# Performance work log

Measured on AMD Instinct MI355X. Metric: run time of the kernel, lower is better.

## Reference

```python
import jax, jax.numpy as jnp
import numpy as np

LABEL_SMOOTHING = 0.1
K_SLOPE = 5.0
N, D = 8192, 256


def setup_inputs() -> dict:
    key = jax.random.key(0)
    k1, k2, k3 = jax.random.split(key, 3)
    return {
        "image_features1": jax.random.normal(k1, (N, D), dtype=jnp.float32),
        "image_features2": jax.random.normal(k2, (N, D), dtype=jnp.float32),
        "logit_scale": jnp.asarray(14.2857, dtype=jnp.float32),  # ~ 1/0.07 CLIP temp
        "positive_weights": jax.random.normal(k3, (N,), dtype=jnp.float32),
    }


def _l2_normalize(x, axis=-1, eps=1e-12):
    # matches F.normalize(dim=-1)
    norm = jnp.linalg.norm(x, axis=axis, keepdims=True)
    return x / jnp.maximum(norm, eps)


def _weighted_infonce(sim, eps):
    # per row i: (1-eps_i)*(-sim[i,i] + lse_i) + eps_i*(-mean(sim[i,:]) + lse_i)
    #          = lse_i - (1-eps_i)*sim[i,i] - eps_i*mean_i
    n = sim.shape[0]
    lse = jax.nn.logsumexp(sim, axis=1)            # [n]
    diag = jnp.diagonal(sim)                       # [n]
    row_mean = jnp.mean(sim, axis=1)               # [n]
    per_row = lse - (1.0 - eps) * diag - eps * row_mean
    return jnp.sum(per_row) / n


def reference(image_features1, image_features2, logit_scale, positive_weights):
    f1 = _l2_normalize(image_features1)
    f2 = _l2_normalize(image_features2)
    logits12 = logit_scale * (f1 @ f2.T)           # [N, N]
    # eps = 1 - (1 - label_smoothing) * sigmoid(k * w)
    eps = 1.0 - (1.0 - LABEL_SMOOTHING) * jax.nn.sigmoid(K_SLOPE * positive_weights)
    loss1 = _weighted_infonce(logits12, eps)
    loss2 = _weighted_infonce(logits12.T, eps)
    return (loss1 + loss2) / 2.0
```

## Files before the change

kernel.cpp:

```cpp
#include <hip/hip_runtime.h>
#include <hip/hip_bf16.h>

#define NN 8192
#define DD 256

typedef __attribute__((ext_vector_type(8))) short short8;
typedef __attribute__((ext_vector_type(4))) float f32x4;

__device__ __forceinline__ unsigned short f2bf(float x) {
    unsigned int u = __float_as_uint(x);
    u += 0x7fff + ((u >> 16) & 1);
    return (unsigned short)(u >> 16);
}
__device__ __forceinline__ float bf2f(unsigned short u) {
    return __uint_as_float(((unsigned int)u) << 16);
}

__global__ __launch_bounds__(256) void nrm_kernel(
    const float* __restrict__ f1, const float* __restrict__ f2,
    const float* __restrict__ scale_p,
    unsigned short* __restrict__ f1n, unsigned short* __restrict__ f2n,
    float* __restrict__ diag)
{
    const int w = threadIdx.x >> 6, lane = threadIdx.x & 63;
    const int row = blockIdx.x * 4 + w;
    const float4 a = reinterpret_cast<const float4*>(f1 + (size_t)row * DD)[lane];
    const float4 b = reinterpret_cast<const float4*>(f2 + (size_t)row * DD)[lane];
    float sa = a.x * a.x + a.y * a.y + a.z * a.z + a.w * a.w;
    float sb = b.x * b.x + b.y * b.y + b.z * b.z + b.w * b.w;
    float sab = a.x * b.x + a.y * b.y + a.z * b.z + a.w * b.w;
#pragma unroll
    for (int off = 1; off < 64; off <<= 1) {
        sa += __shfl_xor(sa, off);
        sb += __shfl_xor(sb, off);
        sab += __shfl_xor(sab, off);
    }
    const float s = scale_p[0];
    const float n1 = fmaxf(sqrtf(sa), 1e-12f);
    const float n2 = fmaxf(sqrtf(sb), 1e-12f);
    if (lane == 0) diag[row] = s * sab / (n1 * n2);
    const float r1 = s / n1, r2 = 1.0f / n2;
    ushort4 o1, o2;
    o1.x = f2bf(a.x * r1); o1.y = f2bf(a.y * r1);
    o1.z = f2bf(a.z * r1); o1.w = f2bf(a.w * r1);
    o2.x = f2bf(b.x * r2); o2.y = f2bf(b.y * r2);
    o2.z = f2bf(b.z * r2); o2.w = f2bf(b.w * r2);
    reinterpret_cast<ushort4*>(f1n + (size_t)row * DD)[lane] = o1;
    reinterpret_cast<ushort4*>(f2n + (size_t)row * DD)[lane] = o2;
}

__global__ __launch_bounds__(256) void sumvec_kernel(
    const unsigned short* __restrict__ f1n, const unsigned short* __restrict__ f2n,
    const float* __restrict__ wts,
    float* __restrict__ S1, float* __restrict__ S2,
    float* __restrict__ T1, float* __restrict__ T2)
{
    __shared__ float epsLds[128];
    const int t = threadIdx.x;
    const int row0 = blockIdx.x * 128;
    if (t < 128)
        epsLds[t] = 1.f - 0.9f / (1.f + __expf(-5.f * wts[row0 + t]));
    __syncthreads();
    const int mat = t >> 7;
    const int half = (t >> 6) & 1;
    const int cg = t & 63;
    const unsigned short* src = (mat ? f2n : f1n) + (size_t)(row0 + half * 64) * DD + cg * 4;
    float s0 = 0, s1 = 0, s2 = 0, s3 = 0, w0 = 0, w1 = 0, w2 = 0, w3 = 0;
    for (int i = 0; i < 64; ++i) {
        const ushort4 v = *reinterpret_cast<const ushort4*>(src + (size_t)i * DD);
        const float e = epsLds[half * 64 + i];
        const float a = bf2f(v.x), b = bf2f(v.y), c = bf2f(v.z), d = bf2f(v.w);
        s0 += a; s1 += b; s2 += c; s3 += d;
        w0 += e * a; w1 += e * b; w2 += e * c; w3 += e * d;
    }
    float* S = mat ? S2 : S1;
    float* T = mat ? T2 : T1;
    atomicAdd(&S[cg * 4 + 0], s0); atomicAdd(&S[cg * 4 + 1], s1);
    atomicAdd(&S[cg * 4 + 2], s2); atomicAdd(&S[cg * 4 + 3], s3);
    atomicAdd(&T[cg * 4 + 0], w0); atomicAdd(&T[cg * 4 + 1], w1);
    atomicAdd(&T[cg * 4 + 2], w2); atomicAdd(&T[cg * 4 + 3], w3);
}

__global__ __launch_bounds__(256, 2) void gemm_kernel(
    const unsigned short* __restrict__ f1n, const unsigned short* __restrict__ f2n,
    float* __restrict__ rowsumexp, float* __restrict__ colsumexp)
{
    __shared__ char Bs[2][64 * 512];
    __shared__ float colbuf[2][1024];
    const int bid = blockIdx.x;
    const int bm = bid >> 3, bc = bid & 7;
    const int w = threadIdx.x >> 6, lane = threadIdx.x & 63;
    const int wr = (w >> 1) * 64, wc = (w & 1) * 32;
    const int lhi = lane >> 4, llo = lane & 15;

    const char* aBase = (const char*)f1n + ((size_t)(bm * 128 + wr + llo) * 512) + lhi * 16;
    short8 av[4][8];
#pragma unroll
    for (int m = 0; m < 4; ++m)
#pragma unroll
        for (int ks = 0; ks < 8; ++ks)
            av[m][ks] = *(const short8*)(aBase + (size_t)(m * 16) * 512 + ks * 64);

    const char* bBase = (const char*)f2n + (size_t)bc * 1024 * 512;

    auto stage = [&](int buf, int tile) {
#pragma unroll
        for (int i = 0; i < 8; ++i) {
            const int r = w * 16 + i * 2 + (lane >> 5);
            const int cs = (lane & 31) ^ (r & 7);
            __builtin_amdgcn_global_load_lds(
                (const __attribute__((address_space(1))) unsigned int*)
                    (bBase + (size_t)(tile * 64 + r) * 512 + cs * 16),
                (__attribute__((address_space(3))) unsigned int*)
                    (&Bs[buf][(w * 16 + i * 2) * 512]), 16, 0, 0);
        }
    };

    float rowpart[16];
#pragma unroll
    for (int i = 0; i < 16; ++i) rowpart[i] = 0.f;

    stage(0, 0);
    __syncthreads();

    for (int t = 0; t < 16; ++t) {
        const int cur = t & 1;
        if (t < 15) stage(cur ^ 1, t + 1);

        f32x4 acc[4][2];
#pragma unroll
        for (int m = 0; m < 4; ++m) {
            acc[m][0] = (f32x4){0.f, 0.f, 0.f, 0.f};
            acc[m][1] = (f32x4){0.f, 0.f, 0.f, 0.f};
        }
        const char* bs = Bs[cur];
#pragma unroll
        for (int ks = 0; ks < 8; ++ks) {
            const int kb = ks * 64 + lhi * 16;
            const int rb0 = wc + llo, rb1 = wc + 16 + llo;
            const short8 bv0 = *(const short8*)(bs + rb0 * 512 + (kb ^ ((rb0 & 7) << 4)));
            const short8 bv1 = *(const short8*)(bs + rb1 * 512 + (kb ^ ((rb1 & 7) << 4)));
#pragma unroll
            for (int m = 0; m < 4; ++m) {
                acc[m][0] = __builtin_amdgcn_mfma_f32_16x16x32_bf16(av[m][ks], bv0, acc[m][0], 0, 0, 0);
                acc[m][1] = __builtin_amdgcn_mfma_f32_16x16x32_bf16(av[m][ks], bv1, acc[m][1], 0, 0, 0);
            }
        }

        float cee0 = 0.f, cee1 = 0.f;
#pragma unroll
        for (int m = 0; m < 4; ++m)
#pragma unroll
            for (int j = 0; j < 4; ++j) {
                const float e0 = __expf(acc[m][0][j]);
                const float e1 = __expf(acc[m][1][j]);
                rowpart[m * 4 + j] += e0 + e1;
                cee0 += e0; cee1 += e1;
            }
        cee0 += __shfl_xor(cee0, 16); cee0 += __shfl_xor(cee0, 32);
        cee1 += __shfl_xor(cee1, 16); cee1 += __shfl_xor(cee1, 32);
        if (lhi == 0) {
            colbuf[w >> 1][t * 64 + wc + llo] = cee0;
            colbuf[w >> 1][t * 64 + wc + 16 + llo] = cee1;
        }
        __syncthreads();
    }

#pragma unroll
    for (int m = 0; m < 4; ++m)
#pragma unroll
        for (int j = 0; j < 4; ++j) {
            float v = rowpart[m * 4 + j];
            v += __shfl_xor(v, 1); v += __shfl_xor(v, 2);
            v += __shfl_xor(v, 4); v += __shfl_xor(v, 8);
            if (llo == 0)
                atomicAdd(&rowsumexp[bm * 128 + wr + m * 16 + lhi * 4 + j], v);
        }
    for (int c = threadIdx.x; c < 1024; c += 256)
        atomicAdd(&colsumexp[bc * 1024 + c], colbuf[0][c] + colbuf[1][c]);
}

__global__ __launch_bounds__(256) void finA_kernel(
    const float* __restrict__ rse, const float* __restrict__ cse,
    const float* __restrict__ diag, const float* __restrict__ wts,
    float* __restrict__ totalp)
{
    const int i = blockIdx.x * 256 + threadIdx.x;
    const float eps = 1.f - 0.9f / (1.f + __expf(-5.f * wts[i]));
    float a = __logf(rse[i]) + __logf(cse[i]) - 2.f * (1.f - eps) * diag[i];
#pragma unroll
    for (int off = 1; off < 64; off <<= 1) a += __shfl_xor(a, off);
    __shared__ float red[4];
    if ((threadIdx.x & 63) == 0) red[threadIdx.x >> 6] = a;
    __syncthreads();
    if (threadIdx.x == 0)
        atomicAdd(totalp, red[0] + red[1] + red[2] + red[3]);
}

__global__ __launch_bounds__(256) void finB_kernel(
    const float* __restrict__ S1, const float* __restrict__ S2,
    const float* __restrict__ T1, const float* __restrict__ T2,
    const float* __restrict__ totalp, float* __restrict__ out)
{
    const int t = threadIdx.x;
    float d = T1[t] * S2[t] + S1[t] * T2[t];
#pragma unroll
    for (int off = 1; off < 64; off <<= 1) d += __shfl_xor(d, off);
    __shared__ float red[4];
    if ((t & 63) == 0) red[t >> 6] = d;
    __syncthreads();
    if (t == 0) {
        const float dot = red[0] + red[1] + red[2] + red[3];
        out[0] = (totalp[0] - dot * (1.f / (float)NN)) * (1.f / (2.f * (float)NN));
    }
}

extern "C" void kernel_launch(void* const* d_in, const int* in_sizes, int n_in,
                              void* d_out, int out_size, void* d_ws, size_t ws_size,
                              hipStream_t stream) {
    (void)in_sizes; (void)n_in; (void)out_size; (void)ws_size;
    const float* f1 = (const float*)d_in[0];
    const float* f2 = (const float*)d_in[1];
    const float* scale = (const float*)d_in[2];
    const float* wts = (const float*)d_in[3];
    float* out = (float*)d_out;

    char* ws = (char*)d_ws;
    unsigned short* f1n = (unsigned short*)ws;
    unsigned short* f2n = (unsigned short*)(ws + (size_t)4 * 1024 * 1024);
    float* fb = (float*)(ws + (size_t)8 * 1024 * 1024);
    float* rse = fb;
    float* cse = fb + 8192;
    float* S1 = fb + 16384;
    float* S2 = fb + 16640;
    float* T1 = fb + 16896;
    float* T2 = fb + 17152;
    float* totalp = fb + 17408;
    float* diag = fb + 18432;

    hipMemsetAsync(fb, 0, (size_t)18432 * sizeof(float), stream);
    nrm_kernel<<<NN / 4, 256, 0, stream>>>(f1, f2, scale, f1n, f2n, diag);
    sumvec_kernel<<<64, 256, 0, stream>>>(f1n, f2n, wts, S1, S2, T1, T2);
    gemm_kernel<<<512, 256, 0, stream>>>(f1n, f2n, rse, cse);
    finA_kernel<<<32, 256, 0, stream>>>(rse, cse, diag, wts, totalp);
    finB_kernel<<<1, 256, 0, stream>>>(S1, S2, T1, T2, totalp, out);
}
```

Baseline: 80.39 us.

## Fuse normalize with column sums, merge finalizers, widen LDS swizzle

Moves the eps-weighted and plain column-sum accumulation into the normalize kernel, computed from fp32 values before the bf16 rounding, and reduces it through LDS. The separate sumvec pass, which re-read the bf16 outputs, is removed. The two finalize kernels become one 1024-thread block, and the large memset shrinks to a 1 KB clear because the normalize kernel now zeroes rse/cse itself. In the GEMM, the B-tile swizzle widens from 8 to 16 chunks to cut LDS bank conflicts, and an empty asm statement pins the A fragments in registers. Risks: fewer blocks in the normalize kernel (256 instead of 2048), and a single-block finalizer that reads all 8192 rows serially.

```diff
diff --git a/kernel.cpp b/kernel.cpp
--- a/kernel.cpp
+++ b/kernel.cpp
@@ -12,73 +12,73 @@
     u += 0x7fff + ((u >> 16) & 1);
     return (unsigned short)(u >> 16);
 }
-__device__ __forceinline__ float bf2f(unsigned short u) {
-    return __uint_as_float(((unsigned int)u) << 16);
-}
 
 __global__ __launch_bounds__(256) void nrm_kernel(
     const float* __restrict__ f1, const float* __restrict__ f2,
-    const float* __restrict__ scale_p,
+    const float* __restrict__ scale_p, const float* __restrict__ wts,
     unsigned short* __restrict__ f1n, unsigned short* __restrict__ f2n,
-    float* __restrict__ diag)
-{
-    const int w = threadIdx.x >> 6, lane = threadIdx.x & 63;
-    const int row = blockIdx.x * 4 + w;
-    const float4 a = reinterpret_cast<const float4*>(f1 + (size_t)row * DD)[lane];
-    const float4 b = reinterpret_cast<const float4*>(f2 + (size_t)row * DD)[lane];
-    float sa = a.x * a.x + a.y * a.y + a.z * a.z + a.w * a.w;
-    float sb = b.x * b.x + b.y * b.y + b.z * b.z + b.w * b.w;
-    float sab = a.x * b.x + a.y * b.y + a.z * b.z + a.w * b.w;
-#pragma unroll
-    for (int off = 1; off < 64; off <<= 1) {
-        sa += __shfl_xor(sa, off);
-        sb += __shfl_xor(sb, off);
-        sab += __shfl_xor(sab, off);
-    }
-    const float s = scale_p[0];
-    const float n1 = fmaxf(sqrtf(sa), 1e-12f);
-    const float n2 = fmaxf(sqrtf(sb), 1e-12f);
-    if (lane == 0) diag[row] = s * sab / (n1 * n2);
-    const float r1 = s / n1, r2 = 1.0f / n2;
-    ushort4 o1, o2;
-    o1.x = f2bf(a.x * r1); o1.y = f2bf(a.y * r1);
-    o1.z = f2bf(a.z * r1); o1.w = f2bf(a.w * r1);
-    o2.x = f2bf(b.x * r2); o2.y = f2bf(b.y * r2);
-    o2.z = f2bf(b.z * r2); o2.w = f2bf(b.w * r2);
-    reinterpret_cast<ushort4*>(f1n + (size_t)row * DD)[lane] = o1;
-    reinterpret_cast<ushort4*>(f2n + (size_t)row * DD)[lane] = o2;
-}
-
-__global__ __launch_bounds__(256) void sumvec_kernel(
-    const unsigned short* __restrict__ f1n, const unsigned short* __restrict__ f2n,
-    const float* __restrict__ wts,
+    float* __restrict__ diag, float* __restrict__ rse, float* __restrict__ cse,
     float* __restrict__ S1, float* __restrict__ S2,
     float* __restrict__ T1, float* __restrict__ T2)
 {
-    __shared__ float epsLds[128];
-    const int t = threadIdx.x;
-    const int row0 = blockIdx.x * 128;
-    if (t < 128)
-        epsLds[t] = 1.f - 0.9f / (1.f + __expf(-5.f * wts[row0 + t]));
+    const int w = threadIdx.x >> 6, lane = threadIdx.x & 63;
+    const int row0 = blockIdx.x * 32 + w * 8;
+    const float s = scale_p[0];
+    float s1a[4] = {0,0,0,0}, t1a[4] = {0,0,0,0};
+    float s2a[4] = {0,0,0,0}, t2a[4] = {0,0,0,0};
+    for (int r = 0; r < 8; ++r) {
+        const int row = row0 + r;
+        const float4 a = reinterpret_cast<const float4*>(f1 + (size_t)row * DD)[lane];
+        const float4 b = reinterpret_cast<const float4*>(f2 + (size_t)row * DD)[lane];
+        float sa = a.x * a.x + a.y * a.y + a.z * a.z + a.w * a.w;
+        float sb = b.x * b.x + b.y * b.y + b.z * b.z + b.w * b.w;
+        float sab = a.x * b.x + a.y * b.y + a.z * b.z + a.w * b.w;
+#pragma unroll
+        for (int off = 1; off < 64; off <<= 1) {
+            sa += __shfl_xor(sa, off);
+            sb += __shfl_xor(sb, off);
+            sab += __shfl_xor(sab, off);
+        }
+        const float n1 = fmaxf(sqrtf(sa), 1e-12f);
+        const float n2 = fmaxf(sqrtf(sb), 1e-12f);
+        const float e = 1.f - 0.9f / (1.f + __expf(-5.f * wts[row]));
+        if (lane == 0) { diag[row] = s * sab / (n1 * n2); rse[row] = 0.f; cse[row] = 0.f; }
+        const float r1 = s / n1, r2 = 1.f / n2;
+        const float v0 = a.x * r1, v1 = a.y * r1, v2 = a.z * r1, v3 = a.w * r1;
+        const float u0 = b.x * r2, u1 = b.y * r2, u2 = b.z * r2, u3 = b.w * r2;
+        ushort4 o1, o2;
+        o1.x = f2bf(v0); o1.y = f2bf(v1); o1.z = f2bf(v2); o1.w = f2bf(v3);
+        o2.x = f2bf(u0); o2.y = f2bf(u1); o2.z = f2bf(u2); o2.w = f2bf(u3);
+        reinterpret_cast<ushort4*>(f1n + (size_t)row * DD)[lane] = o1;
+        reinterpret_cast<ushort4*>(f2n + (size_t)row * DD)[lane] = o2;
+        s1a[0] += v0; s1a[1] += v1; s1a[2] += v2; s1a[3] += v3;
+        t1a[0] += e * v0; t1a[1] += e * v1; t1a[2] += e * v2; t1a[3] += e * v3;
+        s2a[0] += u0; s2a[1] += u1; s2a[2] += u2; s2a[3] += u3;
+        t2a[0] += e * u0; t2a[1] += e * u1; t2a[2] += e * u2; t2a[3] += e * u3;
+    }
+    __shared__ float red[4][64 * 17];
+#pragma unroll
+    for (int k = 0; k < 4; ++k) {
+        red[w][lane * 17 + k]      = s1a[k];
+        red[w][lane * 17 + 4 + k]  = t1a[k];
+        red[w][lane * 17 + 8 + k]  = s2a[k];
+        red[w][lane * 17 + 12 + k] = t2a[k];
+    }
     __syncthreads();
-    const int mat = t >> 7;
-    const int half = (t >> 6) & 1;
-    const int cg = t & 63;
-    const unsigned short* src = (mat ? f2n : f1n) + (size_t)(row0 + half * 64) * DD + cg * 4;
-    float s0 = 0, s1 = 0, s2 = 0, s3 = 0, w0 = 0, w1 = 0, w2 = 0, w3 = 0;
-    for (int i = 0; i < 64; ++i) {
-        const ushort4 v = *reinterpret_cast<const ushort4*>(src + (size_t)i * DD);
-        const float e = epsLds[half * 64 + i];
-        const float a = bf2f(v.x), b = bf2f(v.y), c = bf2f(v.z), d = bf2f(v.w);
-        s0 += a; s1 += b; s2 += c; s3 += d;
-        w0 += e * a; w1 += e * b; w2 += e * c; w3 += e * d;
-    }
-    float* S = mat ? S2 : S1;
-    float* T = mat ? T2 : T1;
-    atomicAdd(&S[cg * 4 + 0], s0); atomicAdd(&S[cg * 4 + 1], s1);
-    atomicAdd(&S[cg * 4 + 2], s2); atomicAdd(&S[cg * 4 + 3], s3);
-    atomicAdd(&T[cg * 4 + 0], w0); atomicAdd(&T[cg * 4 + 1], w1);
-    atomicAdd(&T[cg * 4 + 2], w2); atomicAdd(&T[cg * 4 + 3], w3);
+    {
+        const int ln = threadIdx.x >> 2;
+#pragma unroll
+        for (int q = 0; q < 4; ++q) {
+            const int k = (threadIdx.x & 3) * 4 + q;
+            const float v = red[0][ln * 17 + k] + red[1][ln * 17 + k] +
+                            red[2][ln * 17 + k] + red[3][ln * 17 + k];
+            float* tgt = (k < 4) ? &S1[ln * 4 + k]
+                       : (k < 8) ? &T1[ln * 4 + (k - 4)]
+                       : (k < 12) ? &S2[ln * 4 + (k - 8)]
+                       : &T2[ln * 4 + (k - 12)];
+            atomicAdd(tgt, v);
+        }
+    }
 }
 
 __global__ __launch_bounds__(256, 2) void gemm_kernel(
@@ -100,6 +100,11 @@
 #pragma unroll
         for (int ks = 0; ks < 8; ++ks)
             av[m][ks] = *(const short8*)(aBase + (size_t)(m * 16) * 512 + ks * 64);
+#pragma unroll
+    for (int m = 0; m < 4; ++m)
+#pragma unroll
+        for (int ks = 0; ks < 8; ++ks)
+            asm volatile("" : "+v"(av[m][ks]));
 
     const char* bBase = (const char*)f2n + (size_t)bc * 1024 * 512;
 
@@ -107,7 +112,7 @@
 #pragma unroll
         for (int i = 0; i < 8; ++i) {
             const int r = w * 16 + i * 2 + (lane >> 5);
-            const int cs = (lane & 31) ^ (r & 7);
+            const int cs = (lane & 31) ^ (r & 15);
             __builtin_amdgcn_global_load_lds(
                 (const __attribute__((address_space(1))) unsigned int*)
                     (bBase + (size_t)(tile * 64 + r) * 512 + cs * 16),
@@ -123,6 +128,9 @@
     stage(0, 0);
     __syncthreads();
 
+    const int rb0 = wc + llo, rb1 = wc + 16 + llo;
+    const int sw = llo << 4;
+
     for (int t = 0; t < 16; ++t) {
         const int cur = t & 1;
         if (t < 15) stage(cur ^ 1, t + 1);
@@ -137,9 +145,8 @@
 #pragma unroll
         for (int ks = 0; ks < 8; ++ks) {
             const int kb = ks * 64 + lhi * 16;
-            const int rb0 = wc + llo, rb1 = wc + 16 + llo;
-            const short8 bv0 = *(const short8*)(bs + rb0 * 512 + (kb ^ ((rb0 & 7) << 4)));
-            const short8 bv1 = *(const short8*)(bs + rb1 * 512 + (kb ^ ((rb1 & 7) << 4)));
+            const short8 bv0 = *(const short8*)(bs + rb0 * 512 + (kb ^ sw));
+            const short8 bv1 = *(const short8*)(bs + rb1 * 512 + (kb ^ sw));
 #pragma unroll
             for (int m = 0; m < 4; ++m) {
                 acc[m][0] = __builtin_amdgcn_mfma_f32_16x16x32_bf16(av[m][ks], bv0, acc[m][0], 0, 0, 0);
@@ -180,38 +187,33 @@
         atomicAdd(&colsumexp[bc * 1024 + c], colbuf[0][c] + colbuf[1][c]);
 }
 
-__global__ __launch_bounds__(256) void finA_kernel(
+__global__ __launch_bounds__(1024) void fin_kernel(
     const float* __restrict__ rse, const float* __restrict__ cse,
     const float* __restrict__ diag, const float* __restrict__ wts,
-    float* __restrict__ totalp)
-{
-    const int i = blockIdx.x * 256 + threadIdx.x;
-    const float eps = 1.f - 0.9f / (1.f + __expf(-5.f * wts[i]));
-    float a = __logf(rse[i]) + __logf(cse[i]) - 2.f * (1.f - eps) * diag[i];
-#pragma unroll
-    for (int off = 1; off < 64; off <<= 1) a += __shfl_xor(a, off);
-    __shared__ float red[4];
-    if ((threadIdx.x & 63) == 0) red[threadIdx.x >> 6] = a;
-    __syncthreads();
-    if (threadIdx.x == 0)
-        atomicAdd(totalp, red[0] + red[1] + red[2] + red[3]);
-}
-
-__global__ __launch_bounds__(256) void finB_kernel(
     const float* __restrict__ S1, const float* __restrict__ S2,
     const float* __restrict__ T1, const float* __restrict__ T2,
-    const float* __restrict__ totalp, float* __restrict__ out)
+    float* __restrict__ out)
 {
     const int t = threadIdx.x;
-    float d = T1[t] * S2[t] + S1[t] * T2[t];
-#pragma unroll
-    for (int off = 1; off < 64; off <<= 1) d += __shfl_xor(d, off);
-    __shared__ float red[4];
-    if ((t & 63) == 0) red[t >> 6] = d;
+    float a = 0.f;
+#pragma unroll
+    for (int k = 0; k < 8; ++k) {
+        const int i = t + k * 1024;
+        const float eps = 1.f - 0.9f / (1.f + __expf(-5.f * wts[i]));
+        a += __logf(rse[i]) + __logf(cse[i]) - 2.f * (1.f - eps) * diag[i];
+    }
+    if (t < 256)
+        a -= (T1[t] * S2[t] + S1[t] * T2[t]) * (1.f / (float)NN);
+#pragma unroll
+    for (int off = 1; off < 64; off <<= 1) a += __shfl_xor(a, off);
+    __shared__ float red[16];
+    if ((t & 63) == 0) red[t >> 6] = a;
     __syncthreads();
     if (t == 0) {
-        const float dot = red[0] + red[1] + red[2] + red[3];
-        out[0] = (totalp[0] - dot * (1.f / (float)NN)) * (1.f / (2.f * (float)NN));
+        float tot = 0.f;
+#pragma unroll
+        for (int i = 0; i < 16; ++i) tot += red[i];
+        out[0] = tot * (1.f / (2.f * (float)NN));
     }
 }
 
@@ -229,19 +231,17 @@
     unsigned short* f1n = (unsigned short*)ws;
     unsigned short* f2n = (unsigned short*)(ws + (size_t)4 * 1024 * 1024);
     float* fb = (float*)(ws + (size_t)8 * 1024 * 1024);
-    float* rse = fb;
-    float* cse = fb + 8192;
-    float* S1 = fb + 16384;
-    float* S2 = fb + 16640;
-    float* T1 = fb + 16896;
-    float* T2 = fb + 17152;
-    float* totalp = fb + 17408;
-    float* diag = fb + 18432;
-
-    hipMemsetAsync(fb, 0, (size_t)18432 * sizeof(float), stream);
-    nrm_kernel<<<NN / 4, 256, 0, stream>>>(f1, f2, scale, f1n, f2n, diag);
-    sumvec_kernel<<<64, 256, 0, stream>>>(f1n, f2n, wts, S1, S2, T1, T2);
+    float* rse  = fb;
+    float* cse  = fb + 8192;
+    float* diag = fb + 16384;
+    float* S1   = fb + 24576;
+    float* S2   = fb + 24832;
+    float* T1   = fb + 25088;
+    float* T2   = fb + 25344;
+
+    hipMemsetAsync(S1, 0, 1024 * sizeof(float), stream);
+    nrm_kernel<<<256, 256, 0, stream>>>(f1, f2, scale, wts, f1n, f2n,
+                                        diag, rse, cse, S1, S2, T1, T2);
     gemm_kernel<<<512, 256, 0, stream>>>(f1n, f2n, rse, cse);
-    finA_kernel<<<32, 256, 0, stream>>>(rse, cse, diag, wts, totalp);
-    finB_kernel<<<1, 256, 0, stream>>>(S1, S2, T1, T2, totalp, out);
-}
+    fin_kernel<<<1, 1024, 0, stream>>>(rse, cse, diag, wts, S1, S2, T1, T2, out);
+}
```

Measured after the change: 92.67 us. +15.3%, slower.
